# Kernel optimization log

Hardware: AMD Instinct MI355X
Metric: run time of the kernel (lower is better)

Reference implementation:

```python
import jax, jax.numpy as jnp
import numpy as np

B, C, H = 4, 1, 256          # batch, channels, square image size
A, P = 180, 256              # n_angles, n_detector_positions
T = int(np.ceil(np.sqrt(2.0) * H))  # samples per ray (covers image diagonal) = 363


def setup_inputs() -> dict:
    key = jax.random.key(0)
    x = jax.random.normal(key, (B, C, H, H), dtype=jnp.float32)
    # projection angles uniformly covering [0, pi)
    thetas = (jnp.pi * jnp.arange(A, dtype=jnp.float32) / A)
    # detector offsets in pixel units, centered on the image center
    positions = jnp.arange(P, dtype=jnp.float32) - (P - 1) / 2.0
    return {"x": x, "thetas": thetas, "positions": positions}


def _radon(x, thetas, positions):
    """Radon transform: line integrals along rays (theta, s) with bilinear
    sampling at unit spacing along each ray. Returns sinogram [B,C,A,P]."""
    Bc, Cc, Hh, Ww = x.shape
    cx = (Ww - 1) / 2.0
    cy = (Hh - 1) / 2.0
    t = jnp.arange(T, dtype=x.dtype) - (T - 1) / 2.0          # [T] along-ray param
    cos = jnp.cos(thetas)[:, None, None]                       # [A,1,1]
    sin = jnp.sin(thetas)[:, None, None]
    s = positions[None, :, None]                               # [1,P,1]
    tt = t[None, None, :]                                      # [1,1,T]
    # rotated ray sample coordinates, [A,P,T]
    px = cx + s * cos - tt * sin
    py = cy + s * sin + tt * cos
    x0 = jnp.floor(px)
    y0 = jnp.floor(py)
    wx = px - x0
    wy = py - y0
    x0i = x0.astype(jnp.int32)
    y0i = y0.astype(jnp.int32)

    def gather(iy, ix):
        # zero outside the image (zero-padding boundary)
        valid = (ix >= 0) & (ix < Ww) & (iy >= 0) & (iy < Hh)
        ixc = jnp.clip(ix, 0, Ww - 1)
        iyc = jnp.clip(iy, 0, Hh - 1)
        v = x[:, :, iyc, ixc]                                  # [B,C,A,P,T]
        return v * valid.astype(x.dtype)

    interp = (gather(y0i,     x0i)     * ((1.0 - wx) * (1.0 - wy))
            + gather(y0i,     x0i + 1) * (wx * (1.0 - wy))
            + gather(y0i + 1, x0i)     * ((1.0 - wx) * wy)
            + gather(y0i + 1, x0i + 1) * (wx * wy))
    return interp.sum(axis=-1)                                 # [B,C,A,P]


def reference(x, thetas, positions):
    return _radon(x, thetas, positions)
```

## Files before the change

kernel.cpp:

```cpp
#include <hip/hip_runtime.h>
#include <hip/hip_fp16.h>


#define NB   4
#define NA   180
#define NP   256
#define GANG 3
#define NSEG 4

#define IMG_DW_MAX 17353
#define RED_OFF ((IMG_DW_MAX + 1) * 4)
#define SMEM_BYTES (RED_OFF + NP * NSEG * 4)

template<int STRIDE_DW>
__device__ __forceinline__ float ray_accum(
    const unsigned int* __restrict__ imgw,
    float bxr, float byr, float nsv, float cv,
    float xlo, float xhi, float ylo, float yhi,
    int tlo, int thi, int seg)
{
    float acc = 0.f;
    int   t  = tlo + seg;
    float pxu = fmaf((float)t - 181.0f, nsv, bxr);
    float pyu = fmaf((float)t - 181.0f, cv,  byr);
    const float dpx = 4.0f * nsv;
    const float dpy = 4.0f * cv;
    #pragma unroll 4
    for (; t < thi; t += 4) {
        float px = __builtin_amdgcn_fmed3f(pxu, xlo, xhi);
        float py = __builtin_amdgcn_fmed3f(pyu, ylo, yhi);
        pxu += dpx;
        pyu += dpy;
        const float fx = floorf(px);
        const float fy = floorf(py);
        const float wx = px - fx;
        const float wy = py - fy;
        const int a = (int)fmaf(fy, (float)(2 * STRIDE_DW), fx);
        const int kd = a >> 1;
        const unsigned sh = (a & 1) << 4;
        const unsigned d0 = imgw[kd];
        const unsigned d1 = imgw[kd + 1];
        const unsigned d2 = imgw[kd + STRIDE_DW];
        const unsigned d3 = imgw[kd + STRIDE_DW + 1];
        unsigned q0 = (unsigned)(((((unsigned long long)d1) << 32) | d0) >> sh);
        unsigned q1 = (unsigned)(((((unsigned long long)d3) << 32) | d2) >> sh);
        const __half2 h0 = *reinterpret_cast<__half2*>(&q0);
        const __half2 h1 = *reinterpret_cast<__half2*>(&q1);
        const __half2 dv  = __hsub2(h1, h0);
        const __half2 wy2 = __half2half2(__float2half_rn(wy));
        const __half2 V   = __hfma2(wy2, dv, h0);
        const float vlo = __half2float(__low2half(V));
        const float vhi = __half2float(__high2half(V));
        acc = fmaf(wx, vhi - vlo, acc + vlo);
    }
    return acc;
}

extern "C" __global__ __launch_bounds__(1024)
void radon_fwd(const float* __restrict__ x,
               const float* __restrict__ thetas,
               const float* __restrict__ positions,
               float* __restrict__ out)
{
    extern __shared__ unsigned char smem[];
    unsigned int* imgw = (unsigned int*)smem;
    __half2*      img2 = (__half2*)smem;
    float*        red  = (float*)(smem + RED_OFF);

    const int grp  = blockIdx.x;
    const int b    = blockIdx.y;
    const int half = blockIdx.z;
    const int a0   = grp * GANG;
    const bool regA = (a0 < 45) || (a0 >= 135);
    const int tid = threadIdx.x + (threadIdx.y << 8);
    const float* __restrict__ xb = x + b * 65536;

    for (int i = tid; i <= IMG_DW_MAX; i += 1024) imgw[i] = 0u;
    __syncthreads();

    if (regA) {
        const int rbase  = half ? 126 : 0;
        const int rowoff = half ? 0 : 1;
        const float2* src2 = (const float2*)(xb + rbase * 256);
        for (int j = tid; j < 130 * 128; j += 1024) {
            const int rr = j >> 7;
            const int k  = j & 127;
            float2 v = src2[rr * 128 + k];
            img2[(rr + rowoff) * 131 + k + 1] = __floats2half2_rn(v.x, v.y);
        }
    } else {
        const int cbase2 = half ? 62 : 0;
        const int coff   = half ? 0 : 1;
        const float2* src2 = (const float2*)xb;
        for (int rr = tid >> 6; rr < 256; rr += 16) {
            for (int c2 = tid & 63; c2 < 66; c2 += 64) {
                float2 v = src2[rr * 128 + cbase2 + c2];
                img2[(rr + 1) * 67 + c2 + coff] = __floats2half2_rn(v.x, v.y);
            }
        }
    }
    __syncthreads();

    float xlo, xhi, ylo, yhi;
    if (regA) {
        xlo = 1.f; xhi = 258.f;
        if (half == 0) { ylo = 0.f; yhi = 129.984375f; }
        else           { ylo = 1.f; yhi = 130.f; }
    } else {
        ylo = 0.f; yhi = 257.f;
        if (half == 0) { xlo = 1.f; xhi = 130.984375f; }
        else           { xlo = 3.f; xhi = 132.f; }
    }
    const float rebY = (regA && half) ? 127.f : 0.f;
    const float rebX = (!regA && half) ? 126.f : 0.f;

    const int   p   = threadIdx.x;
    const int   seg = threadIdx.y;
    const float s   = positions[p];

    float accs[GANG];
    for (int g = 0; g < GANG; ++g) {
        const float th  = thetas[a0 + g];
        const float cv  = cosf(th);
        const float sv  = sinf(th);
        const float nsv = -sv;
        const float bx2 = fmaf(s, cv, 129.5f);
        const float by1 = fmaf(s, sv, 128.5f);
        const float slope = regA ? cv : nsv;
        const float base  = regA ? by1 : bx2;
        const float thr   = regA ? 129.f : 130.f;
        const float tstar = 181.0f + (thr - base) / slope;
        const float Sf    = (slope > 0.f) ? ceilf(tstar) : (floorf(tstar) + 1.0f);
        const int   S     = (int)fmaxf(0.f, fminf(364.f, Sf));
        const bool  h0Low = (slope > 0.f);
        int lo, hi;
        if ((half == 0) == h0Low) { lo = 0; hi = S; }
        else                      { lo = S; hi = 364; }

        const float msx = (fabsf(sv) < 1e-7f) ? copysignf(1e-7f, sv) : sv;
        const float mcy = (fabsf(cv) < 1e-7f) ? copysignf(1e-7f, cv) : cv;
        const float invx = -1.0f / msx;
        const float invy =  1.0f / mcy;
        const float ux1 = (1.0f   - bx2) * invx;
        const float ux2 = (258.0f - bx2) * invx;
        const float uy1 = (0.0f   - by1) * invy;
        const float uy2 = (257.0f - by1) * invy;
        const float ulo = fmaxf(fminf(ux1, ux2), fminf(uy1, uy2));
        const float uhi = fminf(fmaxf(ux1, ux2), fmaxf(uy1, uy2));
        const float tbf = ceilf(ulo + 181.0f) - 1.0f;
        const float tef = floorf(uhi + 181.0f) + 2.0f;
        const int tb = (int)fmaxf((float)lo, fminf(364.0f, tbf));
        const int te = (int)fminf((float)hi, fmaxf(0.0f,  tef));

        const float bxr = bx2 - rebX;
        const float byr = by1 - rebY;
        accs[g] = regA
            ? ray_accum<131>(imgw, bxr, byr, nsv, cv, xlo, xhi, ylo, yhi, tb, te, seg)
            : ray_accum< 67>(imgw, bxr, byr, nsv, cv, xlo, xhi, ylo, yhi, tb, te, seg);
    }

    for (int g = 0; g < GANG; ++g) {
        __syncthreads();
        red[(seg << 8) + p] = accs[g];
        __syncthreads();
        if (seg == 0) {
            float r4 = red[p] + red[256 + p] + red[512 + p] + red[768 + p];
            atomicAdd(&out[b * (NA * NP) + (a0 + g) * NP + p], r4);
        }
    }
}

extern "C" void kernel_launch(void* const* d_in, const int* in_sizes, int n_in,
                              void* d_out, int out_size, void* d_ws, size_t ws_size,
                              hipStream_t stream) {
    const float* x         = (const float*)d_in[0];
    const float* thetas    = (const float*)d_in[1];
    const float* positions = (const float*)d_in[2];
    float* out = (float*)d_out;

    hipFuncSetAttribute((const void*)radon_fwd,
                        hipFuncAttributeMaxDynamicSharedMemorySize, SMEM_BYTES);

    hipMemsetAsync(d_out, 0, (size_t)out_size * sizeof(float), stream);

    dim3 grid(NA / GANG, NB, 2);
    dim3 block(NP, NSEG);
    radon_fwd<<<grid, block, SMEM_BYTES, stream>>>(x, thetas, positions, out);
}
```

Baseline: 108.3 us.

## Split image into four strips with vertically-paired half2 layout

Replaces the two-half split with four quarter strips per block, with a shared-memory layout where each dword packs a pixel and the one below it as half2. Each bilinear sample then needs two adjacent dword loads plus byte permutes instead of four loads with 64-bit shifts. The zero-fill pass is dropped because padding is written directly during staging. In exchange the grid doubles, so staging work and atomic adds increase, and the staging loop now uses scalar loads with integer division.

```diff
diff --git a/kernel.cpp b/kernel.cpp
--- a/kernel.cpp
+++ b/kernel.cpp
@@ -7,12 +7,18 @@
 #define NP   256
 #define GANG 3
 #define NSEG 4
+#define NQ   4
 
-#define IMG_DW_MAX 17353
-#define RED_OFF ((IMG_DW_MAX + 1) * 4)
+#define IMG_DW  17802
+#define RED_OFF (IMG_DW * 4)
 #define SMEM_BYTES (RED_OFF + NP * NSEG * 4)
 
-template<int STRIDE_DW>
+__device__ __forceinline__ unsigned pack_h2(float a, float b) {
+    __half2 h = __halves2half2(__float2half_rn(a), __float2half_rn(b));
+    return *reinterpret_cast<unsigned*>(&h);
+}
+
+template<int STRIDE>
 __device__ __forceinline__ float ray_accum(
     const unsigned int* __restrict__ imgw,
     float bxr, float byr, float nsv, float cv,
@@ -35,20 +41,15 @@
         const float fy = floorf(py);
         const float wx = px - fx;
         const float wy = py - fy;
-        const int a = (int)fmaf(fy, (float)(2 * STRIDE_DW), fx);
-        const int kd = a >> 1;
-        const unsigned sh = (a & 1) << 4;
-        const unsigned d0 = imgw[kd];
-        const unsigned d1 = imgw[kd + 1];
-        const unsigned d2 = imgw[kd + STRIDE_DW];
-        const unsigned d3 = imgw[kd + STRIDE_DW + 1];
-        unsigned q0 = (unsigned)(((((unsigned long long)d1) << 32) | d0) >> sh);
-        unsigned q1 = (unsigned)(((((unsigned long long)d3) << 32) | d2) >> sh);
-        const __half2 h0 = *reinterpret_cast<__half2*>(&q0);
-        const __half2 h1 = *reinterpret_cast<__half2*>(&q1);
-        const __half2 dv  = __hsub2(h1, h0);
+        const int ad = (int)fmaf(fy, (float)STRIDE, fx);
+        const unsigned q0 = imgw[ad];
+        const unsigned q1 = imgw[ad + 1];
+        unsigned A = __builtin_amdgcn_perm(q1, q0, 0x05040100u);
+        unsigned B = __builtin_amdgcn_perm(q1, q0, 0x07060302u);
+        const __half2 hA = *reinterpret_cast<__half2*>(&A);
+        const __half2 hB = *reinterpret_cast<__half2*>(&B);
         const __half2 wy2 = __half2half2(__float2half_rn(wy));
-        const __half2 V   = __hfma2(wy2, dv, h0);
+        const __half2 V = __hfma2(wy2, __hsub2(hB, hA), hA);
         const float vlo = __half2float(__low2half(V));
         const float vhi = __half2float(__high2half(V));
         acc = fmaf(wx, vhi - vlo, acc + vlo);
@@ -64,55 +65,42 @@
 {
     extern __shared__ unsigned char smem[];
     unsigned int* imgw = (unsigned int*)smem;
-    __half2*      img2 = (__half2*)smem;
     float*        red  = (float*)(smem + RED_OFF);
 
-    const int grp  = blockIdx.x;
-    const int b    = blockIdx.y;
-    const int half = blockIdx.z;
-    const int a0   = grp * GANG;
+    const int grp = blockIdx.x;
+    const int b   = blockIdx.y;
+    const int qz  = blockIdx.z;
+    const int a0  = grp * GANG;
     const bool regA = (a0 < 45) || (a0 >= 135);
     const int tid = threadIdx.x + (threadIdx.y << 8);
     const float* __restrict__ xb = x + b * 65536;
 
-    for (int i = tid; i <= IMG_DW_MAX; i += 1024) imgw[i] = 0u;
-    __syncthreads();
-
     if (regA) {
-        const int rbase  = half ? 126 : 0;
-        const int rowoff = half ? 0 : 1;
-        const float2* src2 = (const float2*)(xb + rbase * 256);
-        for (int j = tid; j < 130 * 128; j += 1024) {
-            const int rr = j >> 7;
-            const int k  = j & 127;
-            float2 v = src2[rr * 128 + k];
-            img2[(rr + rowoff) * 131 + k + 1] = __floats2half2_rn(v.x, v.y);
+        for (int d = tid; d < 67 * 261; d += 1024) {
+            const int r = d / 261, c = d - r * 261;
+            const int gr = 64 * qz + r - 1;
+            const int gc = c - 2;
+            const bool gok = (gc >= 0) & (gc < 256);
+            const float v0 = (gok && gr >= 0   && gr < 256) ? xb[gr * 256 + gc]       : 0.f;
+            const float v1 = (gok && gr >= -1  && gr < 255) ? xb[(gr + 1) * 256 + gc] : 0.f;
+            imgw[d] = pack_h2(v0, v1);
         }
     } else {
-        const int cbase2 = half ? 62 : 0;
-        const int coff   = half ? 0 : 1;
-        const float2* src2 = (const float2*)xb;
-        for (int rr = tid >> 6; rr < 256; rr += 16) {
-            for (int c2 = tid & 63; c2 < 66; c2 += 64) {
-                float2 v = src2[rr * 128 + cbase2 + c2];
-                img2[(rr + 1) * 67 + c2 + coff] = __floats2half2_rn(v.x, v.y);
-            }
+        for (int d = tid; d < 258 * 69; d += 1024) {
+            const int r = d / 69, c = d - r * 69;
+            const int gr = r - 1;
+            const int gc = 64 * qz + c - 2;
+            const bool gok = (gc >= 0) & (gc < 256);
+            const float v0 = (gok && gr >= 0  && gr < 256) ? xb[gr * 256 + gc]       : 0.f;
+            const float v1 = (gok && gr >= -1 && gr < 255) ? xb[(gr + 1) * 256 + gc] : 0.f;
+            imgw[d] = pack_h2(v0, v1);
         }
     }
     __syncthreads();
 
     float xlo, xhi, ylo, yhi;
-    if (regA) {
-        xlo = 1.f; xhi = 258.f;
-        if (half == 0) { ylo = 0.f; yhi = 129.984375f; }
-        else           { ylo = 1.f; yhi = 130.f; }
-    } else {
-        ylo = 0.f; yhi = 257.f;
-        if (half == 0) { xlo = 1.f; xhi = 130.984375f; }
-        else           { xlo = 3.f; xhi = 132.f; }
-    }
-    const float rebY = (regA && half) ? 127.f : 0.f;
-    const float rebX = (!regA && half) ? 126.f : 0.f;
+    if (regA) { xlo = 1.f; xhi = 258.f;       ylo = 0.f; yhi = 66.f;  }
+    else      { xlo = 1.f; xhi = 66.984375f;  ylo = 0.f; yhi = 257.f; }
 
     const int   p   = threadIdx.x;
     const int   seg = threadIdx.y;
@@ -126,16 +114,26 @@
         const float nsv = -sv;
         const float bx2 = fmaf(s, cv, 129.5f);
         const float by1 = fmaf(s, sv, 128.5f);
+
         const float slope = regA ? cv : nsv;
         const float base  = regA ? by1 : bx2;
-        const float thr   = regA ? 129.f : 130.f;
-        const float tstar = 181.0f + (thr - base) / slope;
-        const float Sf    = (slope > 0.f) ? ceilf(tstar) : (floorf(tstar) + 1.0f);
-        const int   S     = (int)fmaxf(0.f, fminf(364.f, Sf));
-        const bool  h0Low = (slope > 0.f);
+        const float off   = regA ? 1.0f : 2.0f;
+        float S[3];
+        #pragma unroll
+        for (int i = 0; i < 3; ++i) {
+            const float thr = 64.0f * (float)(i + 1) + off;
+            const float ts  = 181.0f + (thr - base) / slope;
+            const float Sf  = (slope > 0.f) ? ceilf(ts) : (floorf(ts) + 1.0f);
+            S[i] = fmaxf(0.f, fminf(364.f, Sf));
+        }
         int lo, hi;
-        if ((half == 0) == h0Low) { lo = 0; hi = S; }
-        else                      { lo = S; hi = 364; }
+        if (slope > 0.f) {
+            lo = (qz == 0) ? 0   : (int)S[qz - 1];
+            hi = (qz == 3) ? 364 : (int)S[qz];
+        } else {
+            lo = (qz == 3) ? 0   : (int)S[qz];
+            hi = (qz == 0) ? 364 : (int)S[qz - 1];
+        }
 
         const float msx = (fabsf(sv) < 1e-7f) ? copysignf(1e-7f, sv) : sv;
         const float mcy = (fabsf(cv) < 1e-7f) ? copysignf(1e-7f, cv) : cv;
@@ -152,11 +150,11 @@
         const int tb = (int)fmaxf((float)lo, fminf(364.0f, tbf));
         const int te = (int)fminf((float)hi, fmaxf(0.0f,  tef));
 
-        const float bxr = bx2 - rebX;
-        const float byr = by1 - rebY;
+        const float bxr = regA ? bx2 : (bx2 - 64.0f * (float)qz);
+        const float byr = regA ? (by1 - 64.0f * (float)qz) : by1;
         accs[g] = regA
-            ? ray_accum<131>(imgw, bxr, byr, nsv, cv, xlo, xhi, ylo, yhi, tb, te, seg)
-            : ray_accum< 67>(imgw, bxr, byr, nsv, cv, xlo, xhi, ylo, yhi, tb, te, seg);
+            ? ray_accum<261>(imgw, bxr, byr, nsv, cv, xlo, xhi, ylo, yhi, tb, te, seg)
+            : ray_accum< 69>(imgw, bxr, byr, nsv, cv, xlo, xhi, ylo, yhi, tb, te, seg);
     }
 
     for (int g = 0; g < GANG; ++g) {
@@ -183,7 +181,7 @@
 
     hipMemsetAsync(d_out, 0, (size_t)out_size * sizeof(float), stream);
 
-    dim3 grid(NA / GANG, NB, 2);
+    dim3 grid(NA / GANG, NB, NQ);
     dim3 block(NP, NSEG);
     radon_fwd<<<grid, block, SMEM_BYTES, stream>>>(x, thetas, positions, out);
 }
```

New measurement: 125.6 us. +16.0%, slower.

## Interleave ray segments within wavefronts and reduce via shuffles instead of LDS

Applied to the files above, without the earlier changes.

Remaps threads so the four t-segments of each detector position sit in adjacent lanes of one wavefront, and replaces the shared-memory reduction buffer and its block-wide barriers with two xor shuffles. This removes the per-angle __syncthreads pairs and the LDS reduction area, which shrinks shared memory use. Neighbouring lanes now sample interleaved points along the same ray, which changes the LDS access pattern and lane divergence over the per-ray t bounds.

```diff
diff --git a/kernel.cpp b/kernel.cpp
--- a/kernel.cpp
+++ b/kernel.cpp
@@ -6,11 +6,13 @@
 #define NA   180
 #define NP   256
 #define GANG 3
-#define NSEG 4
+#define IMG_DW_MAX 17353
+#define SMEM_BYTES ((IMG_DW_MAX + 1) * 4)
 
-#define IMG_DW_MAX 17353
-#define RED_OFF ((IMG_DW_MAX + 1) * 4)
-#define SMEM_BYTES (RED_OFF + NP * NSEG * 4)
+__device__ __forceinline__ unsigned pack_h2(float a, float b) {
+    __half2 h = __halves2half2(__float2half_rn(a), __float2half_rn(b));
+    return *reinterpret_cast<unsigned*>(&h);
+}
 
 template<int STRIDE_DW>
 __device__ __forceinline__ float ray_accum(
@@ -35,7 +37,7 @@
         const float fy = floorf(py);
         const float wx = px - fx;
         const float wy = py - fy;
-        const int a = (int)fmaf(fy, (float)(2 * STRIDE_DW), fx);
+        const int a  = (int)fmaf(fy, (float)(2 * STRIDE_DW), fx);
         const int kd = a >> 1;
         const unsigned sh = (a & 1) << 4;
         const unsigned d0 = imgw[kd];
@@ -64,15 +66,13 @@
 {
     extern __shared__ unsigned char smem[];
     unsigned int* imgw = (unsigned int*)smem;
-    __half2*      img2 = (__half2*)smem;
-    float*        red  = (float*)(smem + RED_OFF);
 
     const int grp  = blockIdx.x;
     const int b    = blockIdx.y;
     const int half = blockIdx.z;
     const int a0   = grp * GANG;
     const bool regA = (a0 < 45) || (a0 >= 135);
-    const int tid = threadIdx.x + (threadIdx.y << 8);
+    const int tid = threadIdx.x;
     const float* __restrict__ xb = x + b * 65536;
 
     for (int i = tid; i <= IMG_DW_MAX; i += 1024) imgw[i] = 0u;
@@ -86,7 +86,7 @@
             const int rr = j >> 7;
             const int k  = j & 127;
             float2 v = src2[rr * 128 + k];
-            img2[(rr + rowoff) * 131 + k + 1] = __floats2half2_rn(v.x, v.y);
+            imgw[(rr + rowoff) * 131 + k + 1] = pack_h2(v.x, v.y);
         }
     } else {
         const int cbase2 = half ? 62 : 0;
@@ -95,7 +95,7 @@
         for (int rr = tid >> 6; rr < 256; rr += 16) {
             for (int c2 = tid & 63; c2 < 66; c2 += 64) {
                 float2 v = src2[rr * 128 + cbase2 + c2];
-                img2[(rr + 1) * 67 + c2 + coff] = __floats2half2_rn(v.x, v.y);
+                imgw[(rr + 1) * 67 + c2 + coff] = pack_h2(v.x, v.y);
             }
         }
     }
@@ -114,11 +114,11 @@
     const float rebY = (regA && half) ? 127.f : 0.f;
     const float rebX = (!regA && half) ? 126.f : 0.f;
 
-    const int   p   = threadIdx.x;
-    const int   seg = threadIdx.y;
-    const float s   = positions[p];
+    const int lane = tid & 63;
+    const int seg  = lane & 3;
+    const int p    = ((tid >> 6) << 4) + (lane >> 2);
+    const float s  = positions[p];
 
-    float accs[GANG];
     for (int g = 0; g < GANG; ++g) {
         const float th  = thetas[a0 + g];
         const float cv  = cosf(th);
@@ -133,9 +133,8 @@
         const float Sf    = (slope > 0.f) ? ceilf(tstar) : (floorf(tstar) + 1.0f);
         const int   S     = (int)fmaxf(0.f, fminf(364.f, Sf));
         const bool  h0Low = (slope > 0.f);
-        int lo, hi;
-        if ((half == 0) == h0Low) { lo = 0; hi = S; }
-        else                      { lo = S; hi = 364; }
+        const int lo = ((half == 0) == h0Low) ? 0 : S;
+        const int hi = ((half == 0) == h0Low) ? S : 364;
 
         const float msx = (fabsf(sv) < 1e-7f) ? copysignf(1e-7f, sv) : sv;
         const float mcy = (fabsf(cv) < 1e-7f) ? copysignf(1e-7f, cv) : cv;
@@ -154,19 +153,14 @@
 
         const float bxr = bx2 - rebX;
         const float byr = by1 - rebY;
-        accs[g] = regA
+        float acc = regA
             ? ray_accum<131>(imgw, bxr, byr, nsv, cv, xlo, xhi, ylo, yhi, tb, te, seg)
             : ray_accum< 67>(imgw, bxr, byr, nsv, cv, xlo, xhi, ylo, yhi, tb, te, seg);
-    }
 
-    for (int g = 0; g < GANG; ++g) {
-        __syncthreads();
-        red[(seg << 8) + p] = accs[g];
-        __syncthreads();
-        if (seg == 0) {
-            float r4 = red[p] + red[256 + p] + red[512 + p] + red[768 + p];
-            atomicAdd(&out[b * (NA * NP) + (a0 + g) * NP + p], r4);
-        }
+        acc += __shfl_xor(acc, 1, 64);
+        acc += __shfl_xor(acc, 2, 64);
+        if (seg == 0)
+            atomicAdd(&out[b * (NA * NP) + (a0 + g) * NP + p], acc);
     }
 }
 
@@ -184,6 +178,6 @@
     hipMemsetAsync(d_out, 0, (size_t)out_size * sizeof(float), stream);
 
     dim3 grid(NA / GANG, NB, 2);
-    dim3 block(NP, NSEG);
+    dim3 block(1024);
     radon_fwd<<<grid, block, SMEM_BYTES, stream>>>(x, thetas, positions, out);
 }
```

Result: faster. 104.8 us (-3.2%).
